# Kernel tuning notes

Measured on AMD Instinct MI355X. Metric: run time of the kernel, lower is better.

The kernel has to match this reference:

```python
import jax, jax.numpy as jnp
import numpy as np

B, L, C, H, W = 2, 4, 64, 80, 80
DISCRETE_RATIO, DOWNSAMPLE_RATE, NUM_ITER = 0.4, 2, 2


def _conv2d(x, w, b):
    y = jax.lax.conv_general_dilated(x, w, (1, 1), 'SAME',
                                     dimension_numbers=('NCHW', 'OIHW', 'NCHW'))
    return y + b[None, :, None, None]


def _get_transformation_matrix(M, h, w):
    # shift(center) @ [R 0; 0 1] @ shift(-center), then add raw translation (kornia-style)
    R = M[:, :2, :2]
    center = jnp.array([w / 2.0, h / 2.0], M.dtype)
    trans = center[None, :] - jnp.einsum('nij,j->ni', R, center) + M[:, :, 2]
    return jnp.concatenate([R, trans[:, :, None]], axis=2)  # (N,2,3)


def _warp_affine(src, M, mode):
    # src (N,C,h,w); M (N,2,3) maps src pixels -> dst pixels; sample src at M^{-1} @ dst
    # (equivalent to F.affine_grid/grid_sample with align_corners=True, zeros padding)
    N, Cc, h, w = src.shape
    bottom = jnp.tile(jnp.array([[[0.0, 0.0, 1.0]]], src.dtype), (N, 1, 1))
    Minv = jnp.linalg.inv(jnp.concatenate([M, bottom], axis=1))
    yy, xx = jnp.meshgrid(jnp.arange(h, dtype=src.dtype),
                          jnp.arange(w, dtype=src.dtype), indexing='ij')
    pts = jnp.stack([xx.ravel(), yy.ravel(), jnp.ones(h * w, src.dtype)], 0)  # (3,P)
    sp = jnp.einsum('nij,jp->nip', Minv, pts)
    sx, sy = sp[:, 0], sp[:, 1]  # (N,P) source pixel coords
    flat = src.reshape(N, Cc, h * w)

    def gather(ix, iy):
        valid = ((ix >= 0) & (ix < w) & (iy >= 0) & (iy < h)).astype(src.dtype)
        idx = jnp.clip(iy, 0, h - 1) * w + jnp.clip(ix, 0, w - 1)
        vals = jnp.take_along_axis(flat, jnp.broadcast_to(idx[:, None, :], (N, Cc, h * w)), axis=2)
        return vals * valid[:, None, :]

    if mode == 'nearest':
        out = gather(jnp.round(sx).astype(jnp.int32), jnp.round(sy).astype(jnp.int32))
    else:
        x0 = jnp.floor(sx); y0 = jnp.floor(sy)
        fx = (sx - x0)[:, None, :]; fy = (sy - y0)[:, None, :]
        x0 = x0.astype(jnp.int32); y0 = y0.astype(jnp.int32)
        out = (gather(x0, y0) * (1 - fx) * (1 - fy)
               + gather(x0 + 1, y0) * fx * (1 - fy)
               + gather(x0, y0 + 1) * (1 - fx) * fy
               + gather(x0 + 1, y0 + 1) * fx * fy)
    return out.reshape(N, Cc, h, w)


def _forward(x, pairwise_t_matrix, msg_w, msg_b, gates_w, gates_b, can_w, can_b, mlp_w, mlp_b):
    feats = x.reshape(B, L, C, H, W)
    # rows [0,1], cols [0,1,3] of the 4x4 SE(3) matrices; discretize translation
    t = pairwise_t_matrix[..., :2, :][..., jnp.array([0, 1, 3])]  # (B,L,L,2,3)
    t = t.at[..., 2].set(t[..., 2] / (DISCRETE_RATIO * DOWNSAMPLE_RATE))
    T = _get_transformation_matrix(t.reshape(-1, 2, 3), H, W)  # (B*L*L,2,3), flat index (b, j, i)
    mask = _warp_affine(jnp.ones((B * L * L, 1, H, W), x.dtype), T, 'nearest').reshape(B, L, L, 1, H, W)

    for _ in range(NUM_ITER):
        # 'b c h w -> b c w h' + flip(last): coordinate-convention fix (H==W)
        y = jnp.flip(jnp.swapaxes(feats, -1, -2), axis=-1)  # (B,L,C,H,W)
        # warp neighbor j into ego i frame with T[b,j,i]
        src = jnp.broadcast_to(y[:, :, None], (B, L, L, C, H, W)).reshape(-1, C, H, W)
        neighbor = _warp_affine(src, T, 'bilinear')
        ego = jnp.broadcast_to(y[:, None], (B, L, L, C, H, W)).reshape(-1, C, H, W)
        msg = _conv2d(jnp.concatenate([neighbor, ego], axis=1), msg_w, msg_b)
        msg = msg.reshape(B, L, L, C, H, W) * mask
        agg = msg.mean(axis=1)  # 'avg' over neighbors j -> (B,L,C,H,W)
        cat_feat = jnp.concatenate([y, agg], axis=2).reshape(B * L, 2 * C, H, W)
        # single ConvGRU step with zero initial hidden state
        h0 = jnp.zeros((B * L, C, H, W), x.dtype)
        gates = _conv2d(jnp.concatenate([cat_feat, h0], axis=1), gates_w, gates_b)
        reset = jax.nn.sigmoid(gates[:, :C])
        update = jax.nn.sigmoid(gates[:, C:])
        cand = jnp.tanh(_conv2d(jnp.concatenate([cat_feat, reset * h0], axis=1), can_w, can_b))
        h1 = (1.0 - update) * h0 + update * cand
        # undo the coordinate fix: flip(last) then 'c w h -> c h w'
        feats = jnp.swapaxes(jnp.flip(h1.reshape(B, L, C, H, W), axis=-1), -1, -2)

    out = feats[:, 0]  # ego agent of each sample, (B,C,H,W)
    return jnp.einsum('bchw,oc->bhwo', out, mlp_w) + mlp_b  # nn.Linear on channel-last


def setup_inputs() -> dict:
    key = jax.random.key(0)
    ks = jax.random.split(key, 12)
    x = jax.random.normal(ks[0], (B * L, C, H, W), dtype=jnp.float32)
    record_len = jnp.full((B,), L, dtype=jnp.int32)
    # realistic SE(2) pairwise transforms embedded in 4x4 homogeneous matrices
    ang = jax.random.uniform(ks[1], (B, L, L), minval=-0.3, maxval=0.3)
    tx = jax.random.uniform(ks[2], (B, L, L), minval=-8.0, maxval=8.0)
    ty = jax.random.uniform(ks[3], (B, L, L), minval=-8.0, maxval=8.0)
    c, s = jnp.cos(ang), jnp.sin(ang)
    z, o = jnp.zeros_like(ang), jnp.ones_like(ang)
    pairwise_t_matrix = jnp.stack([c, -s, z, tx,
                                   s, c, z, ty,
                                   z, z, o, z,
                                   z, z, z, o], axis=-1).reshape(B, L, L, 4, 4).astype(jnp.float32)
    prior_encoding = jax.random.normal(ks[4], (B * L, 3), dtype=jnp.float32)  # unused by forward
    sc = 0.05
    return {
        'x': x,
        'record_len': record_len,
        'pairwise_t_matrix': pairwise_t_matrix,
        'prior_encoding': prior_encoding,
        'msg_w': jax.random.normal(ks[5], (C, 2 * C, 3, 3), dtype=jnp.float32) * sc,
        'msg_b': jnp.zeros((C,), jnp.float32),
        'gates_w': jax.random.normal(ks[6], (2 * C, 3 * C, 3, 3), dtype=jnp.float32) * sc,
        'gates_b': jnp.zeros((2 * C,), jnp.float32),
        'can_w': jax.random.normal(ks[7], (C, 3 * C, 3, 3), dtype=jnp.float32) * sc,
        'can_b': jnp.zeros((C,), jnp.float32),
        'mlp_w': jax.random.normal(ks[8], (C, C), dtype=jnp.float32) * sc,
        'mlp_b': jnp.zeros((C,), jnp.float32),
    }


def reference(x, record_len, pairwise_t_matrix, prior_encoding,
              msg_w, msg_b, gates_w, gates_b, can_w, can_b, mlp_w, mlp_b):
    # record_len is fixed to L for every sample; prior_encoding is unused by the torch forward
    return _forward(x, pairwise_t_matrix, msg_w, msg_b, gates_w, gates_b,
                    can_w, can_b, mlp_w, mlp_b)
```

## Files before the change

kernel.cpp:

```cpp
#include <hip/hip_runtime.h>
#include <math.h>

#define WD 80
#define HW 6400
#define PW 82
#define PPX 6790
#define NIMG 8
#define NPAIR 32
#define RR 2
#define STG 640

typedef short bf16x8 __attribute__((ext_vector_type(8)));
typedef float f32x4 __attribute__((ext_vector_type(4)));

__device__ __forceinline__ float bf2f(unsigned short u) {
    return __uint_as_float(((unsigned)u) << 16);
}
__device__ __forceinline__ unsigned short f2bf(float f) {
    unsigned u = __float_as_uint(f);
    u += 0x7fff + ((u >> 16) & 1);
    return (unsigned short)(u >> 16);
}

__device__ __forceinline__ void inv_affine(const float* __restrict__ P, int p, float* a) {
    const float* m = P + p * 16;
    float m00 = m[0], m01 = m[1], m02 = m[3] / 0.8f;
    float m10 = m[4], m11 = m[5], m12 = m[7] / 0.8f;
    float cx = 40.0f, cy = 40.0f;
    float tx = cx - (m00 * cx + m01 * cy) + m02;
    float ty = cy - (m10 * cx + m11 * cy) + m12;
    float id = 1.0f / (m00 * m11 - m01 * m10);
    a[0] =  m11 * id; a[1] = -m01 * id;
    a[3] = -m10 * id; a[4] =  m00 * id;
    a[2] = -(a[0] * tx + a[1] * ty);
    a[5] = -(a[3] * tx + a[4] * ty);
}

__global__ void make_mask2(const float* __restrict__ P, float* __restrict__ mats,
                           float* __restrict__ mask) {
    int p = blockIdx.x;
    float a[6];
    inv_affine(P, p, a);
    if (threadIdx.x < 6) mats[p * 6 + threadIdx.x] = a[threadIdx.x];
    for (int q = threadIdx.x; q < HW; q += blockDim.x) {
        float x = (float)(q % WD), y = (float)(q / WD);
        float sx = a[0] * x + a[1] * y + a[2];
        float sy = a[3] * x + a[4] * y + a[5];
        int ix = (int)rintf(sx), iy = (int)rintf(sy);
        mask[p * HW + q] = (ix >= 0 && ix < WD && iy >= 0 && iy < WD) ? 1.0f : 0.0f;
    }
}

__global__ void zero_u4(uint4* __restrict__ p, int n4) {
    int t = blockIdx.x * blockDim.x + threadIdx.x;
    if (t < n4) p[t] = (uint4){0, 0, 0, 0};
}

__global__ __launch_bounds__(256) void rot_init_t(const float* __restrict__ x,
                                                  unsigned short* __restrict__ Y) {
    __shared__ float T[64][81];
    int img = blockIdx.x / 80, hh = blockIdx.x % 80;
    int tid = threadIdx.x;
    for (int idx = tid; idx < 64 * 80; idx += 256) {
        int c = idx / 80, ww = idx % 80;
        T[c][ww] = x[((size_t)(img * 64 + c) * 80 + hh) * 80 + ww];
    }
    __syncthreads();
    int b = 79 - hh;
    for (int idx = tid; idx < 80 * 64; idx += 256) {
        int a = idx >> 6, ch = idx & 63;
        Y[((size_t)img * PPX + (a + 1) * PW + (b + 1)) * 64 + ch] = f2bf(T[ch][a]);
    }
}

__global__ void prep_w_all(const float* __restrict__ msg_w, const float* __restrict__ gates_w,
                           const float* __restrict__ can_w,
                           unsigned short* __restrict__ Wn, unsigned short* __restrict__ We,
                           unsigned short* __restrict__ Wu, unsigned short* __restrict__ Wc) {
    int t = blockIdx.x * blockDim.x + threadIdx.x;
    if (t >= 221184) return;
    const float* src; unsigned short* dst;
    int cin_n, co_off, ci_off, stride, u;
    if (t < 36864)       { src = msg_w;   dst = Wn; cin_n = 64;  co_off = 0;  ci_off = 0;  stride = 1152; u = t; }
    else if (t < 73728)  { src = msg_w;   dst = We; cin_n = 64;  co_off = 0;  ci_off = 64; stride = 1152; u = t - 36864; }
    else if (t < 147456) { src = gates_w; dst = Wu; cin_n = 128; co_off = 64; ci_off = 0;  stride = 1728; u = t - 73728; }
    else                 { src = can_w;   dst = Wc; cin_n = 128; co_off = 0;  ci_off = 0;  stride = 1728; u = t - 147456; }
    int ci = u % cin_n;
    int co = (u / cin_n) & 63;
    int tap = u / (cin_n * 64);
    dst[u] = f2bf(src[(size_t)(co_off + co) * stride + (ci_off + ci) * 9 + tap]);
}

__global__ void warp_pairs(const unsigned short* __restrict__ Ysrc, const float* __restrict__ mats,
                           unsigned short* __restrict__ warped, int total, int only0) {
    int idx = blockIdx.x * blockDim.x + threadIdx.x;
    if (idx >= total) return;
    int g = idx & 7;
    int pp = (idx >> 3) % 6724;
    int k = idx / (6724 * 8);
    int p = only0 ? k * 4 : k;
    int py = pp / PW, pxx = pp % PW;
    uint4 v = {0, 0, 0, 0};
    if (py >= 1 && py <= 80 && pxx >= 1 && pxx <= 80) {
        int y = py - 1, x = pxx - 1;
        const float* a = mats + p * 6;
        float sx = a[0] * x + a[1] * y + a[2];
        float sy = a[3] * x + a[4] * y + a[5];
        float fxf = floorf(sx), fyf = floorf(sy);
        float fx = sx - fxf, fy = sy - fyf;
        int ix = (int)fxf, iy = (int)fyf;
        float w00 = (1.f - fx) * (1.f - fy), w10 = fx * (1.f - fy);
        float w01 = (1.f - fx) * fy,         w11 = fx * fy;
        bool vx0 = (unsigned)ix < WD, vx1 = (unsigned)(ix + 1) < WD;
        bool vy0 = (unsigned)iy < WD, vy1 = (unsigned)(iy + 1) < WD;
        if (!(vx0 && vy0)) w00 = 0.f;
        if (!(vx1 && vy0)) w10 = 0.f;
        if (!(vx0 && vy1)) w01 = 0.f;
        if (!(vx1 && vy1)) w11 = 0.f;
        int cx0 = min(max(ix, 0), WD - 1), cx1 = min(max(ix + 1, 0), WD - 1);
        int cy0 = min(max(iy, 0), WD - 1), cy1 = min(max(iy + 1, 0), WD - 1);
        const unsigned short* src = Ysrc + (size_t)(p >> 2) * PPX * 64 + g * 8;
        uint4 c00 = *(const uint4*)(src + ((cy0 + 1) * PW + cx0 + 1) * 64);
        uint4 c10 = *(const uint4*)(src + ((cy0 + 1) * PW + cx1 + 1) * 64);
        uint4 c01 = *(const uint4*)(src + ((cy1 + 1) * PW + cx0 + 1) * 64);
        uint4 c11 = *(const uint4*)(src + ((cy1 + 1) * PW + cx1 + 1) * 64);
        const unsigned short* p00 = (const unsigned short*)&c00;
        const unsigned short* p10 = (const unsigned short*)&c10;
        const unsigned short* p01 = (const unsigned short*)&c01;
        const unsigned short* p11 = (const unsigned short*)&c11;
        unsigned short r8[8];
#pragma unroll
        for (int kk = 0; kk < 8; ++kk) {
            float vv = w00 * bf2f(p00[kk]) + w10 * bf2f(p10[kk])
                     + w01 * bf2f(p01[kk]) + w11 * bf2f(p11[kk]);
            r8[kk] = f2bf(vv);
        }
        v = *(const uint4*)r8;
    }
    *(uint4*)(warped + ((size_t)k * PPX + pp) * 64 + g * 8) = v;
}

__device__ __forceinline__ void stage_t(const unsigned short* __restrict__ src,
                                        int x0, int y0, uint4* bufbase, int tid) {
    const int lane = tid & 63;
    const int wv = tid >> 6;
    for (int c = wv; c < STG / 64; c += 4) {
        int s = c * 64 + lane;
        int q = s >> 3;
        int yl = q / 20, xl = q - yl * 20;
        int g = (s & 7) ^ (q & 7);
        const unsigned short* gp = src + ((y0 + yl) * PW + x0 + xl) * 64 + g * 8;
        __builtin_amdgcn_global_load_lds(
            (const __attribute__((address_space(1))) unsigned int*)gp,
            (__attribute__((address_space(3))) unsigned int*)(bufbase + c * 64),
            16, 0, 0);
    }
}

__device__ __forceinline__ void load_w(const unsigned short* __restrict__ W, int row,
                                       int cinstride, int cin0, int lh, bf16x8* Wf) {
#pragma unroll
    for (int ks = 0; ks < 2; ++ks)
#pragma unroll
        for (int tap = 0; tap < 9; ++tap)
            Wf[ks * 9 + tap] = *(const bf16x8*)(W + (size_t)(tap * 64 + row) * cinstride
                                                + cin0 + ks * 32 + lh * 8);
}

__device__ __forceinline__ void conv_pass(const uint4* __restrict__ buf, const bf16x8* Wf,
                                          int ll, int lh, f32x4* acc) {
#pragma unroll
    for (int ks = 0; ks < 2; ++ks) {
        int g = ks * 4 + lh;
#pragma unroll
        for (int tap = 0; tap < 9; ++tap) {
            bf16x8 B = Wf[ks * 9 + tap];
            int ty = tap / 3, tx = tap % 3;
#pragma unroll
            for (int r = 0; r < RR; ++r) {
                int q = (r + ty) * 20 + tx + ll;
                bf16x8 A = *(const bf16x8*)&buf[q * 8 + (g ^ (q & 7))];
                acc[r] = __builtin_amdgcn_mfma_f32_16x16x32_bf16(A, B, acc[r], 0, 0, 0);
            }
        }
    }
}

__global__ __launch_bounds__(256) void msg_agg(const unsigned short* __restrict__ warped,
        const unsigned short* __restrict__ Y, const float* __restrict__ mask,
        const unsigned short* __restrict__ Wn, const unsigned short* __restrict__ We,
        const float* __restrict__ bias, unsigned short* __restrict__ Gpad, int only0) {
    __shared__ uint4 lds[2 * STG];
    __shared__ float lmask[4][RR][16];
    const int tid = threadIdx.x, lane = tid & 63, wv = tid >> 6;
    const int ll = lane & 15, lh = lane >> 4;
    const int x0 = blockIdx.x * 16, y0 = blockIdx.y * RR;
    const int t = blockIdx.z;
    const int b = only0 ? t : (t >> 2), j = only0 ? 0 : (t & 3);
    const int row = wv * 16 + ll;
    const int img = only0 ? t * 4 : t;

    int ks_[4];
#pragma unroll
    for (int i = 0; i < 4; ++i)
        ks_[i] = only0 ? (b * 4 + i) : ((b * 4 + i) * 4 + j);
    if (tid < 4 * RR * 16) {
        int i = tid / (RR * 16), r = (tid >> 4) % RR, px = tid & 15;
        int p = only0 ? ks_[i] * 4 : ks_[i];
        lmask[i][r][px] = mask[(size_t)p * HW + (y0 + r) * WD + x0 + px];
    }
    bf16x8 Wf[18];
    load_w(Wn, row, 64, 0, lh, Wf);
    stage_t(warped + (size_t)ks_[0] * PPX * 64, x0, y0, lds, tid);
    __syncthreads();

    f32x4 tot[RR];
#pragma unroll
    for (int r = 0; r < RR; ++r) tot[r] = (f32x4){0.f, 0.f, 0.f, 0.f};

    for (int i = 0; i < 4; ++i) {
        if (i < 3)
            stage_t(warped + (size_t)ks_[i + 1] * PPX * 64, x0, y0, lds + ((i + 1) & 1) * STG, tid);
        else
            stage_t(Y + (size_t)img * PPX * 64, x0, y0, lds, tid);
        f32x4 acc[RR];
#pragma unroll
        for (int r = 0; r < RR; ++r) acc[r] = (f32x4){0.f, 0.f, 0.f, 0.f};
        conv_pass(lds + (i & 1) * STG, Wf, ll, lh, acc);
#pragma unroll
        for (int r = 0; r < RR; ++r)
#pragma unroll
            for (int jj = 0; jj < 4; ++jj)
                tot[r][jj] += lmask[i][r][lh * 4 + jj] * acc[r][jj];
        __syncthreads();
    }

    load_w(We, row, 64, 0, lh, Wf);
    f32x4 acc[RR];
#pragma unroll
    for (int r = 0; r < RR; ++r) acc[r] = (f32x4){0.f, 0.f, 0.f, 0.f};
    conv_pass(lds, Wf, ll, lh, acc);

    float bv = bias[row];
#pragma unroll
    for (int r = 0; r < RR; ++r)
#pragma unroll
        for (int jj = 0; jj < 4; ++jj) {
            int px = lh * 4 + jj;
            float msum = lmask[0][r][px] + lmask[1][r][px] + lmask[2][r][px] + lmask[3][r][px];
            float val = 0.25f * (tot[r][jj] + msum * (acc[r][jj] + bv));
            Gpad[((size_t)t * PPX + (y0 + r + 1) * PW + (x0 + px + 1)) * 64 + row] = f2bf(val);
        }
}

__global__ __launch_bounds__(256) void gru_conv(const unsigned short* __restrict__ Ysrc,
        const unsigned short* __restrict__ Gpad,
        const unsigned short* __restrict__ Wu, const unsigned short* __restrict__ Wc,
        const float* __restrict__ bu, const float* __restrict__ bc,
        unsigned short* __restrict__ Ydst, int only0) {
    __shared__ uint4 lds[2 * STG];
    const int tid = threadIdx.x, lane = tid & 63, wv = tid >> 6;
    const int ll = lane & 15, lh = lane >> 4;
    const int x0 = blockIdx.x * 16, y0 = blockIdx.y * RR;
    const int t = blockIdx.z;
    const int img = only0 ? t * 4 : t;
    const int row = wv * 16 + ll;

    stage_t(Ysrc + (size_t)img * PPX * 64, x0, y0, lds, tid);
    stage_t(Gpad + (size_t)t * PPX * 64, x0, y0, lds + STG, tid);
    bf16x8 Wf[18];
    load_w(Wu, row, 128, 0, lh, Wf);
    __syncthreads();

    f32x4 aU[RR], aC[RR];
#pragma unroll
    for (int r = 0; r < RR; ++r) {
        aU[r] = (f32x4){0.f, 0.f, 0.f, 0.f};
        aC[r] = (f32x4){0.f, 0.f, 0.f, 0.f};
    }
    conv_pass(lds, Wf, ll, lh, aU);
    load_w(Wu, row, 128, 64, lh, Wf);
    conv_pass(lds + STG, Wf, ll, lh, aU);
    load_w(Wc, row, 128, 0, lh, Wf);
    conv_pass(lds, Wf, ll, lh, aC);
    load_w(Wc, row, 128, 64, lh, Wf);
    conv_pass(lds + STG, Wf, ll, lh, aC);

    float ub = bu[row], cb = bc[row];
#pragma unroll
    for (int r = 0; r < RR; ++r)
#pragma unroll
        for (int jj = 0; jj < 4; ++jj) {
            float u = 1.f / (1.f + __expf(-(aU[r][jj] + ub)));
            float e2 = __expf(2.f * (aC[r][jj] + cb));
            float c = (e2 - 1.f) / (e2 + 1.f);
            Ydst[((size_t)img * PPX + (y0 + r + 1) * PW + (x0 + lh * 4 + jj + 1)) * 64 + row]
                = f2bf(u * c);
        }
}

__global__ void final_mlp(const unsigned short* __restrict__ yfin, const float* __restrict__ mw,
                          const float* __restrict__ mb, float* __restrict__ out) {
    int t = blockIdx.x * blockDim.x + threadIdx.x;
    if (t >= 2 * HW * 64) return;
    int o  = t & 63;
    int wv = (t >> 6) % WD;
    int h  = ((t >> 6) / WD) % WD;
    int b  = t / (HW * 64);
    const unsigned short* src = yfin + ((size_t)(b * 4) * PPX + (wv + 1) * PW + (80 - h)) * 64;
    const float* wrow = mw + o * 64;
    float r = mb[o];
#pragma unroll
    for (int c8 = 0; c8 < 8; ++c8) {
        bf16x8 v = *(const bf16x8*)(src + c8 * 8);
#pragma unroll
        for (int k = 0; k < 8; ++k)
            r += bf2f(((const unsigned short*)&v)[k]) * wrow[c8 * 8 + k];
    }
    out[t] = r;
}

extern "C" void kernel_launch(void* const* d_in, const int* in_sizes, int n_in,
                              void* d_out, int out_size, void* d_ws, size_t ws_size,
                              hipStream_t stream) {
    const float* x       = (const float*)d_in[0];
    const float* P       = (const float*)d_in[2];
    const float* msg_w   = (const float*)d_in[4];
    const float* msg_b   = (const float*)d_in[5];
    const float* gates_w = (const float*)d_in[6];
    const float* gates_b = (const float*)d_in[7];
    const float* can_w   = (const float*)d_in[8];
    const float* can_b   = (const float*)d_in[9];
    const float* mlp_w   = (const float*)d_in[10];
    const float* mlp_b   = (const float*)d_in[11];
    float* out = (float*)d_out;

    char* wsb = (char*)d_ws;
    float* mats = (float*)wsb;
    float* mask = (float*)(wsb + 1024);
    unsigned short* Wn = (unsigned short*)(wsb + 820224);
    unsigned short* We = Wn + 36864;
    unsigned short* Wu = We + 36864;
    unsigned short* Wc = Wu + 73728;
    unsigned short* Y0 = Wc + 73728;
    unsigned short* Y1 = Y0 + (size_t)NIMG * PPX * 64;
    unsigned short* Gpad = Y1 + (size_t)NIMG * PPX * 64;
    unsigned short* warped = Gpad + (size_t)NIMG * PPX * 64;

    {
        int n4 = (int)((size_t)3 * NIMG * PPX * 64 * 2 / 16);
        zero_u4<<<(n4 + 255) / 256, 256, 0, stream>>>((uint4*)Y0, n4);
    }
    make_mask2<<<NPAIR, 256, 0, stream>>>(P, mats, mask);
    prep_w_all<<<(221184 + 255) / 256, 256, 0, stream>>>(msg_w, gates_w, can_w, Wn, We, Wu, Wc);
    rot_init_t<<<NIMG * 80, 256, 0, stream>>>(x, Y0);

    warp_pairs<<<(32 * 6724 * 8 + 255) / 256, 256, 0, stream>>>(Y0, mats, warped, 32 * 6724 * 8, 0);
    msg_agg<<<dim3(5, 80 / RR, 8), 256, 0, stream>>>(warped, Y0, mask, Wn, We, msg_b, Gpad, 0);
    gru_conv<<<dim3(5, 80 / RR, 8), 256, 0, stream>>>(Y0, Gpad, Wu, Wc, gates_b + 64, can_b, Y1, 0);

    warp_pairs<<<(8 * 6724 * 8 + 255) / 256, 256, 0, stream>>>(Y1, mats, warped, 8 * 6724 * 8, 1);
    msg_agg<<<dim3(5, 80 / RR, 2), 256, 0, stream>>>(warped, Y1, mask, Wn, We, msg_b, Gpad, 1);
    gru_conv<<<dim3(5, 80 / RR, 2), 256, 0, stream>>>(Y1, Gpad, Wu, Wc, gates_b + 64, can_b, Y0, 1);

    final_mlp<<<(2 * HW * 64 + 255) / 256, 256, 0, stream>>>(Y0, mlp_w, mlp_b, out);
}
```

Measured before the change: 282.6 us.

## Enlarge conv tiles to 8 rows with warp row/channel split and A-fragment reuse

The conv kernels now process 8 output rows per block instead of 2. Each wave computes 4 rows by 32 output channels, and each loaded A fragment is reused across the 3 vertical taps and 2 channel groups. Weights are read from global/L1 inside the loop instead of being held in registers. This cuts halo restaging and LDS reads per output. The trade-offs are 4x fewer blocks (200 or 50 per launch), larger LDS usage, and more global weight loads in the inner loop.

```diff
diff --git a/kernel.cpp b/kernel.cpp
--- a/kernel.cpp
+++ b/kernel.cpp
@@ -7,8 +7,8 @@
 #define PPX 6790
 #define NIMG 8
 #define NPAIR 32
-#define RR 2
-#define STG 640
+#define YR 8
+#define TSTG 1600
 
 typedef short bf16x8 __attribute__((ext_vector_type(8)));
 typedef float f32x4 __attribute__((ext_vector_type(4)));
@@ -144,7 +144,7 @@
                                         int x0, int y0, uint4* bufbase, int tid) {
     const int lane = tid & 63;
     const int wv = tid >> 6;
-    for (int c = wv; c < STG / 64; c += 4) {
+    for (int c = wv; c < TSTG / 64; c += 4) {
         int s = c * 64 + lane;
         int q = s >> 3;
         int yl = q / 20, xl = q - yl * 20;
@@ -157,146 +157,168 @@
     }
 }
 
-__device__ __forceinline__ void load_w(const unsigned short* __restrict__ W, int row,
-                                       int cinstride, int cin0, int lh, bf16x8* Wf) {
-#pragma unroll
-    for (int ks = 0; ks < 2; ++ks)
-#pragma unroll
-        for (int tap = 0; tap < 9; ++tap)
-            Wf[ks * 9 + tap] = *(const bf16x8*)(W + (size_t)(tap * 64 + row) * cinstride
+__device__ __forceinline__ void conv_pass(const uint4* __restrict__ buf,
+        const unsigned short* __restrict__ W, int cinstride, int cin0,
+        int ll, int lh, int rg, int cgp, f32x4 acc[2][4]) {
+#pragma unroll
+    for (int ks = 0; ks < 2; ++ks) {
+        const int g = ks * 4 + lh;
+#pragma unroll
+        for (int tx = 0; tx < 3; ++tx) {
+            bf16x8 A[6];
+#pragma unroll
+            for (int s = 0; s < 6; ++s) {
+                int q = (rg * 4 + s) * 20 + tx + ll;
+                A[s] = *(const bf16x8*)&buf[q * 8 + (g ^ (q & 7))];
+            }
+#pragma unroll
+            for (int ty = 0; ty < 3; ++ty) {
+                int tap = ty * 3 + tx;
+#pragma unroll
+                for (int c2 = 0; c2 < 2; ++c2) {
+                    int co = cgp * 32 + c2 * 16 + ll;
+                    bf16x8 B = *(const bf16x8*)(W + (size_t)(tap * 64 + co) * cinstride
                                                 + cin0 + ks * 32 + lh * 8);
-}
-
-__device__ __forceinline__ void conv_pass(const uint4* __restrict__ buf, const bf16x8* Wf,
-                                          int ll, int lh, f32x4* acc) {
-#pragma unroll
-    for (int ks = 0; ks < 2; ++ks) {
-        int g = ks * 4 + lh;
-#pragma unroll
-        for (int tap = 0; tap < 9; ++tap) {
-            bf16x8 B = Wf[ks * 9 + tap];
-            int ty = tap / 3, tx = tap % 3;
-#pragma unroll
-            for (int r = 0; r < RR; ++r) {
-                int q = (r + ty) * 20 + tx + ll;
-                bf16x8 A = *(const bf16x8*)&buf[q * 8 + (g ^ (q & 7))];
-                acc[r] = __builtin_amdgcn_mfma_f32_16x16x32_bf16(A, B, acc[r], 0, 0, 0);
-            }
-        }
-    }
-}
-
-__global__ __launch_bounds__(256) void msg_agg(const unsigned short* __restrict__ warped,
+#pragma unroll
+                    for (int r = 0; r < 4; ++r)
+                        acc[c2][r] = __builtin_amdgcn_mfma_f32_16x16x32_bf16(A[r + ty], B, acc[c2][r], 0, 0, 0);
+                }
+            }
+        }
+    }
+}
+
+__global__ __launch_bounds__(256, 3) void msg_agg(const unsigned short* __restrict__ warped,
         const unsigned short* __restrict__ Y, const float* __restrict__ mask,
         const unsigned short* __restrict__ Wn, const unsigned short* __restrict__ We,
         const float* __restrict__ bias, unsigned short* __restrict__ Gpad, int only0) {
-    __shared__ uint4 lds[2 * STG];
-    __shared__ float lmask[4][RR][16];
+    __shared__ uint4 lds[2 * TSTG];
+    __shared__ float lmask[4][YR][16];
     const int tid = threadIdx.x, lane = tid & 63, wv = tid >> 6;
     const int ll = lane & 15, lh = lane >> 4;
-    const int x0 = blockIdx.x * 16, y0 = blockIdx.y * RR;
+    const int rg = wv & 1, cgp = wv >> 1;
+    const int x0 = blockIdx.x * 16, y0 = blockIdx.y * YR;
     const int t = blockIdx.z;
     const int b = only0 ? t : (t >> 2), j = only0 ? 0 : (t & 3);
-    const int row = wv * 16 + ll;
     const int img = only0 ? t * 4 : t;
 
     int ks_[4];
 #pragma unroll
     for (int i = 0; i < 4; ++i)
         ks_[i] = only0 ? (b * 4 + i) : ((b * 4 + i) * 4 + j);
-    if (tid < 4 * RR * 16) {
-        int i = tid / (RR * 16), r = (tid >> 4) % RR, px = tid & 15;
+    for (int idx = tid; idx < 4 * YR * 16; idx += 256) {
+        int i = idx / (YR * 16), r = (idx >> 4) % YR, px = idx & 15;
         int p = only0 ? ks_[i] * 4 : ks_[i];
         lmask[i][r][px] = mask[(size_t)p * HW + (y0 + r) * WD + x0 + px];
     }
-    bf16x8 Wf[18];
-    load_w(Wn, row, 64, 0, lh, Wf);
     stage_t(warped + (size_t)ks_[0] * PPX * 64, x0, y0, lds, tid);
     __syncthreads();
 
-    f32x4 tot[RR];
-#pragma unroll
-    for (int r = 0; r < RR; ++r) tot[r] = (f32x4){0.f, 0.f, 0.f, 0.f};
+    f32x4 tot[2][4];
+    float msum[4][4];
+#pragma unroll
+    for (int c2 = 0; c2 < 2; ++c2)
+#pragma unroll
+        for (int r = 0; r < 4; ++r) tot[c2][r] = (f32x4){0.f, 0.f, 0.f, 0.f};
+#pragma unroll
+    for (int r = 0; r < 4; ++r)
+#pragma unroll
+        for (int jj = 0; jj < 4; ++jj) msum[r][jj] = 0.f;
 
     for (int i = 0; i < 4; ++i) {
         if (i < 3)
-            stage_t(warped + (size_t)ks_[i + 1] * PPX * 64, x0, y0, lds + ((i + 1) & 1) * STG, tid);
+            stage_t(warped + (size_t)ks_[i + 1] * PPX * 64, x0, y0, lds + ((i + 1) & 1) * TSTG, tid);
         else
             stage_t(Y + (size_t)img * PPX * 64, x0, y0, lds, tid);
-        f32x4 acc[RR];
-#pragma unroll
-        for (int r = 0; r < RR; ++r) acc[r] = (f32x4){0.f, 0.f, 0.f, 0.f};
-        conv_pass(lds + (i & 1) * STG, Wf, ll, lh, acc);
-#pragma unroll
-        for (int r = 0; r < RR; ++r)
-#pragma unroll
-            for (int jj = 0; jj < 4; ++jj)
-                tot[r][jj] += lmask[i][r][lh * 4 + jj] * acc[r][jj];
+        f32x4 acc[2][4];
+#pragma unroll
+        for (int c2 = 0; c2 < 2; ++c2)
+#pragma unroll
+            for (int r = 0; r < 4; ++r) acc[c2][r] = (f32x4){0.f, 0.f, 0.f, 0.f};
+        conv_pass(lds + (i & 1) * TSTG, Wn, 64, 0, ll, lh, rg, cgp, acc);
+#pragma unroll
+        for (int r = 0; r < 4; ++r)
+#pragma unroll
+            for (int jj = 0; jj < 4; ++jj) {
+                float m = lmask[i][rg * 4 + r][lh * 4 + jj];
+                msum[r][jj] += m;
+#pragma unroll
+                for (int c2 = 0; c2 < 2; ++c2) tot[c2][r][jj] += m * acc[c2][r][jj];
+            }
         __syncthreads();
     }
 
-    load_w(We, row, 64, 0, lh, Wf);
-    f32x4 acc[RR];
-#pragma unroll
-    for (int r = 0; r < RR; ++r) acc[r] = (f32x4){0.f, 0.f, 0.f, 0.f};
-    conv_pass(lds, Wf, ll, lh, acc);
-
-    float bv = bias[row];
-#pragma unroll
-    for (int r = 0; r < RR; ++r)
-#pragma unroll
-        for (int jj = 0; jj < 4; ++jj) {
-            int px = lh * 4 + jj;
-            float msum = lmask[0][r][px] + lmask[1][r][px] + lmask[2][r][px] + lmask[3][r][px];
-            float val = 0.25f * (tot[r][jj] + msum * (acc[r][jj] + bv));
-            Gpad[((size_t)t * PPX + (y0 + r + 1) * PW + (x0 + px + 1)) * 64 + row] = f2bf(val);
-        }
-}
-
-__global__ __launch_bounds__(256) void gru_conv(const unsigned short* __restrict__ Ysrc,
+    f32x4 acc[2][4];
+#pragma unroll
+    for (int c2 = 0; c2 < 2; ++c2)
+#pragma unroll
+        for (int r = 0; r < 4; ++r) acc[c2][r] = (f32x4){0.f, 0.f, 0.f, 0.f};
+    conv_pass(lds, We, 64, 0, ll, lh, rg, cgp, acc);
+
+#pragma unroll
+    for (int c2 = 0; c2 < 2; ++c2) {
+        int co = cgp * 32 + c2 * 16 + ll;
+        float bv = bias[co];
+#pragma unroll
+        for (int r = 0; r < 4; ++r) {
+            int y = y0 + rg * 4 + r;
+#pragma unroll
+            for (int jj = 0; jj < 4; ++jj) {
+                int x = x0 + lh * 4 + jj;
+                float val = 0.25f * (tot[c2][r][jj] + msum[r][jj] * (acc[c2][r][jj] + bv));
+                Gpad[((size_t)t * PPX + (y + 1) * PW + (x + 1)) * 64 + co] = f2bf(val);
+            }
+        }
+    }
+}
+
+__global__ __launch_bounds__(256, 3) void gru_conv(const unsigned short* __restrict__ Ysrc,
         const unsigned short* __restrict__ Gpad,
         const unsigned short* __restrict__ Wu, const unsigned short* __restrict__ Wc,
         const float* __restrict__ bu, const float* __restrict__ bc,
         unsigned short* __restrict__ Ydst, int only0) {
-    __shared__ uint4 lds[2 * STG];
+    __shared__ uint4 lds[2 * TSTG];
     const int tid = threadIdx.x, lane = tid & 63, wv = tid >> 6;
     const int ll = lane & 15, lh = lane >> 4;
-    const int x0 = blockIdx.x * 16, y0 = blockIdx.y * RR;
+    const int rg = wv & 1, cgp = wv >> 1;
+    const int x0 = blockIdx.x * 16, y0 = blockIdx.y * YR;
     const int t = blockIdx.z;
     const int img = only0 ? t * 4 : t;
-    const int row = wv * 16 + ll;
 
     stage_t(Ysrc + (size_t)img * PPX * 64, x0, y0, lds, tid);
-    stage_t(Gpad + (size_t)t * PPX * 64, x0, y0, lds + STG, tid);
-    bf16x8 Wf[18];
-    load_w(Wu, row, 128, 0, lh, Wf);
+    stage_t(Gpad + (size_t)t * PPX * 64, x0, y0, lds + TSTG, tid);
     __syncthreads();
 
-    f32x4 aU[RR], aC[RR];
-#pragma unroll
-    for (int r = 0; r < RR; ++r) {
-        aU[r] = (f32x4){0.f, 0.f, 0.f, 0.f};
-        aC[r] = (f32x4){0.f, 0.f, 0.f, 0.f};
-    }
-    conv_pass(lds, Wf, ll, lh, aU);
-    load_w(Wu, row, 128, 64, lh, Wf);
-    conv_pass(lds + STG, Wf, ll, lh, aU);
-    load_w(Wc, row, 128, 0, lh, Wf);
-    conv_pass(lds, Wf, ll, lh, aC);
-    load_w(Wc, row, 128, 64, lh, Wf);
-    conv_pass(lds + STG, Wf, ll, lh, aC);
-
-    float ub = bu[row], cb = bc[row];
-#pragma unroll
-    for (int r = 0; r < RR; ++r)
-#pragma unroll
-        for (int jj = 0; jj < 4; ++jj) {
-            float u = 1.f / (1.f + __expf(-(aU[r][jj] + ub)));
-            float e2 = __expf(2.f * (aC[r][jj] + cb));
-            float c = (e2 - 1.f) / (e2 + 1.f);
-            Ydst[((size_t)img * PPX + (y0 + r + 1) * PW + (x0 + lh * 4 + jj + 1)) * 64 + row]
-                = f2bf(u * c);
-        }
+    f32x4 aU[2][4], aC[2][4];
+#pragma unroll
+    for (int c2 = 0; c2 < 2; ++c2)
+#pragma unroll
+        for (int r = 0; r < 4; ++r) {
+            aU[c2][r] = (f32x4){0.f, 0.f, 0.f, 0.f};
+            aC[c2][r] = (f32x4){0.f, 0.f, 0.f, 0.f};
+        }
+    conv_pass(lds,        Wu, 128, 0,  ll, lh, rg, cgp, aU);
+    conv_pass(lds + TSTG, Wu, 128, 64, ll, lh, rg, cgp, aU);
+    conv_pass(lds,        Wc, 128, 0,  ll, lh, rg, cgp, aC);
+    conv_pass(lds + TSTG, Wc, 128, 64, ll, lh, rg, cgp, aC);
+
+#pragma unroll
+    for (int c2 = 0; c2 < 2; ++c2) {
+        int co = cgp * 32 + c2 * 16 + ll;
+        float ub = bu[co], cb = bc[co];
+#pragma unroll
+        for (int r = 0; r < 4; ++r) {
+            int y = y0 + rg * 4 + r;
+#pragma unroll
+            for (int jj = 0; jj < 4; ++jj) {
+                int x = x0 + lh * 4 + jj;
+                float u = 1.f / (1.f + __expf(-(aU[c2][r][jj] + ub)));
+                float e2 = __expf(2.f * (aC[c2][r][jj] + cb));
+                float c = (e2 - 1.f) / (e2 + 1.f);
+                Ydst[((size_t)img * PPX + (y + 1) * PW + (x + 1)) * 64 + co] = f2bf(u * c);
+            }
+        }
+    }
 }
 
 __global__ void final_mlp(const unsigned short* __restrict__ yfin, const float* __restrict__ mw,
@@ -356,12 +378,12 @@
     rot_init_t<<<NIMG * 80, 256, 0, stream>>>(x, Y0);
 
     warp_pairs<<<(32 * 6724 * 8 + 255) / 256, 256, 0, stream>>>(Y0, mats, warped, 32 * 6724 * 8, 0);
-    msg_agg<<<dim3(5, 80 / RR, 8), 256, 0, stream>>>(warped, Y0, mask, Wn, We, msg_b, Gpad, 0);
-    gru_conv<<<dim3(5, 80 / RR, 8), 256, 0, stream>>>(Y0, Gpad, Wu, Wc, gates_b + 64, can_b, Y1, 0);
+    msg_agg<<<dim3(5, 80 / YR, 8), 256, 0, stream>>>(warped, Y0, mask, Wn, We, msg_b, Gpad, 0);
+    gru_conv<<<dim3(5, 80 / YR, 8), 256, 0, stream>>>(Y0, Gpad, Wu, Wc, gates_b + 64, can_b, Y1, 0);
 
     warp_pairs<<<(8 * 6724 * 8 + 255) / 256, 256, 0, stream>>>(Y1, mats, warped, 8 * 6724 * 8, 1);
-    msg_agg<<<dim3(5, 80 / RR, 2), 256, 0, stream>>>(warped, Y1, mask, Wn, We, msg_b, Gpad, 1);
-    gru_conv<<<dim3(5, 80 / RR, 2), 256, 0, stream>>>(Y1, Gpad, Wu, Wc, gates_b + 64, can_b, Y0, 1);
+    msg_agg<<<dim3(5, 80 / YR, 2), 256, 0, stream>>>(warped, Y1, mask, Wn, We, msg_b, Gpad, 1);
+    gru_conv<<<dim3(5, 80 / YR, 2), 256, 0, stream>>>(Y1, Gpad, Wu, Wc, gates_b + 64, can_b, Y0, 1);
 
     final_mlp<<<(2 * HW * 64 + 255) / 256, 256, 0, stream>>>(Y0, mlp_w, mlp_b, out);
 }
```

New measurement: 395.1 us. 1.4x slower.

## Enlarge conv tiles to four rows with register-reused A fragments and fused prologue

Applied to the files above, without the earlier changes.

Each conv block now covers four output rows instead of two, and staged LDS tiles grow to match. The inner loop loads six A fragments per column tap and reuses each across the three row taps, which cuts LDS reads per MFMA. gru_conv double-buffers its weight fragments so the next weight load overlaps the current pass. The mask and weight-prep kernels are merged into one prologue launch, and both conv kernels get a launch bound of two blocks per SIMD. In exchange there are half as many blocks, which may lower occupancy and latency hiding, and register pressure rises.

```diff
diff --git a/kernel.cpp b/kernel.cpp
--- a/kernel.cpp
+++ b/kernel.cpp
@@ -7,8 +7,7 @@
 #define PPX 6790
 #define NIMG 8
 #define NPAIR 32
-#define RR 2
-#define STG 640
+#define TSTG 960
 
 typedef short bf16x8 __attribute__((ext_vector_type(8)));
 typedef float f32x4 __attribute__((ext_vector_type(4)));
@@ -36,48 +35,28 @@
     a[5] = -(a[3] * tx + a[4] * ty);
 }
 
-__global__ void make_mask2(const float* __restrict__ P, float* __restrict__ mats,
-                           float* __restrict__ mask) {
-    int p = blockIdx.x;
-    float a[6];
-    inv_affine(P, p, a);
-    if (threadIdx.x < 6) mats[p * 6 + threadIdx.x] = a[threadIdx.x];
-    for (int q = threadIdx.x; q < HW; q += blockDim.x) {
-        float x = (float)(q % WD), y = (float)(q / WD);
-        float sx = a[0] * x + a[1] * y + a[2];
-        float sy = a[3] * x + a[4] * y + a[5];
-        int ix = (int)rintf(sx), iy = (int)rintf(sy);
-        mask[p * HW + q] = (ix >= 0 && ix < WD && iy >= 0 && iy < WD) ? 1.0f : 0.0f;
-    }
-}
-
-__global__ void zero_u4(uint4* __restrict__ p, int n4) {
-    int t = blockIdx.x * blockDim.x + threadIdx.x;
-    if (t < n4) p[t] = (uint4){0, 0, 0, 0};
-}
-
-__global__ __launch_bounds__(256) void rot_init_t(const float* __restrict__ x,
-                                                  unsigned short* __restrict__ Y) {
-    __shared__ float T[64][81];
-    int img = blockIdx.x / 80, hh = blockIdx.x % 80;
-    int tid = threadIdx.x;
-    for (int idx = tid; idx < 64 * 80; idx += 256) {
-        int c = idx / 80, ww = idx % 80;
-        T[c][ww] = x[((size_t)(img * 64 + c) * 80 + hh) * 80 + ww];
-    }
-    __syncthreads();
-    int b = 79 - hh;
-    for (int idx = tid; idx < 80 * 64; idx += 256) {
-        int a = idx >> 6, ch = idx & 63;
-        Y[((size_t)img * PPX + (a + 1) * PW + (b + 1)) * 64 + ch] = f2bf(T[ch][a]);
-    }
-}
-
-__global__ void prep_w_all(const float* __restrict__ msg_w, const float* __restrict__ gates_w,
-                           const float* __restrict__ can_w,
-                           unsigned short* __restrict__ Wn, unsigned short* __restrict__ We,
-                           unsigned short* __restrict__ Wu, unsigned short* __restrict__ Wc) {
-    int t = blockIdx.x * blockDim.x + threadIdx.x;
+__global__ void prologue(const float* __restrict__ P, float* __restrict__ mats,
+                         float* __restrict__ mask,
+                         const float* __restrict__ msg_w, const float* __restrict__ gates_w,
+                         const float* __restrict__ can_w,
+                         unsigned short* __restrict__ Wn, unsigned short* __restrict__ We,
+                         unsigned short* __restrict__ Wu, unsigned short* __restrict__ Wc) {
+    int bx = blockIdx.x;
+    if (bx < 32) {
+        int p = bx;
+        float a[6];
+        inv_affine(P, p, a);
+        if (threadIdx.x < 6) mats[p * 6 + threadIdx.x] = a[threadIdx.x];
+        for (int q = threadIdx.x; q < HW; q += blockDim.x) {
+            float x = (float)(q % WD), y = (float)(q / WD);
+            float sx = a[0] * x + a[1] * y + a[2];
+            float sy = a[3] * x + a[4] * y + a[5];
+            int ix = (int)rintf(sx), iy = (int)rintf(sy);
+            mask[p * HW + q] = (ix >= 0 && ix < WD && iy >= 0 && iy < WD) ? 1.0f : 0.0f;
+        }
+        return;
+    }
+    int t = (bx - 32) * 256 + threadIdx.x;
     if (t >= 221184) return;
     const float* src; unsigned short* dst;
     int cin_n, co_off, ci_off, stride, u;
@@ -89,6 +68,28 @@
     int co = (u / cin_n) & 63;
     int tap = u / (cin_n * 64);
     dst[u] = f2bf(src[(size_t)(co_off + co) * stride + (ci_off + ci) * 9 + tap]);
+}
+
+__global__ void zero_u4(uint4* __restrict__ p, int n4) {
+    int t = blockIdx.x * blockDim.x + threadIdx.x;
+    if (t < n4) p[t] = (uint4){0, 0, 0, 0};
+}
+
+__global__ __launch_bounds__(256) void rot_init_t(const float* __restrict__ x,
+                                                  unsigned short* __restrict__ Y) {
+    __shared__ float T[64][81];
+    int img = blockIdx.x / 80, hh = blockIdx.x % 80;
+    int tid = threadIdx.x;
+    for (int idx = tid; idx < 64 * 80; idx += 256) {
+        int c = idx / 80, ww = idx % 80;
+        T[c][ww] = x[((size_t)(img * 64 + c) * 80 + hh) * 80 + ww];
+    }
+    __syncthreads();
+    int b = 79 - hh;
+    for (int idx = tid; idx < 80 * 64; idx += 256) {
+        int a = idx >> 6, ch = idx & 63;
+        Y[((size_t)img * PPX + (a + 1) * PW + (b + 1)) * 64 + ch] = f2bf(T[ch][a]);
+    }
 }
 
 __global__ void warp_pairs(const unsigned short* __restrict__ Ysrc, const float* __restrict__ mats,
@@ -144,7 +145,7 @@
                                         int x0, int y0, uint4* bufbase, int tid) {
     const int lane = tid & 63;
     const int wv = tid >> 6;
-    for (int c = wv; c < STG / 64; c += 4) {
+    for (int c = wv; c < TSTG / 64; c += 4) {
         int s = c * 64 + lane;
         int q = s >> 3;
         int yl = q / 20, xl = q - yl * 20;
@@ -167,45 +168,50 @@
                                                 + cin0 + ks * 32 + lh * 8);
 }
 
-__device__ __forceinline__ void conv_pass(const uint4* __restrict__ buf, const bf16x8* Wf,
-                                          int ll, int lh, f32x4* acc) {
+__device__ __forceinline__ void conv_pass4(const uint4* __restrict__ buf, const bf16x8* Wf,
+                                           int ll, int lh, f32x4* acc) {
 #pragma unroll
     for (int ks = 0; ks < 2; ++ks) {
-        int g = ks * 4 + lh;
-#pragma unroll
-        for (int tap = 0; tap < 9; ++tap) {
-            bf16x8 B = Wf[ks * 9 + tap];
-            int ty = tap / 3, tx = tap % 3;
-#pragma unroll
-            for (int r = 0; r < RR; ++r) {
-                int q = (r + ty) * 20 + tx + ll;
-                bf16x8 A = *(const bf16x8*)&buf[q * 8 + (g ^ (q & 7))];
-                acc[r] = __builtin_amdgcn_mfma_f32_16x16x32_bf16(A, B, acc[r], 0, 0, 0);
+        const int g = ks * 4 + lh;
+#pragma unroll
+        for (int tx = 0; tx < 3; ++tx) {
+            bf16x8 A[6];
+#pragma unroll
+            for (int s = 0; s < 6; ++s) {
+                int q = s * 20 + tx + ll;
+                A[s] = *(const bf16x8*)&buf[q * 8 + (g ^ (q & 7))];
             }
-        }
-    }
-}
-
-__global__ __launch_bounds__(256) void msg_agg(const unsigned short* __restrict__ warped,
+#pragma unroll
+            for (int ty = 0; ty < 3; ++ty) {
+                bf16x8 B = Wf[ks * 9 + ty * 3 + tx];
+#pragma unroll
+                for (int r = 0; r < 4; ++r)
+                    acc[r] = __builtin_amdgcn_mfma_f32_16x16x32_bf16(A[r + ty], B, acc[r], 0, 0, 0);
+            }
+        }
+    }
+}
+
+__global__ __launch_bounds__(256, 2) void msg_agg(const unsigned short* __restrict__ warped,
         const unsigned short* __restrict__ Y, const float* __restrict__ mask,
         const unsigned short* __restrict__ Wn, const unsigned short* __restrict__ We,
         const float* __restrict__ bias, unsigned short* __restrict__ Gpad, int only0) {
-    __shared__ uint4 lds[2 * STG];
-    __shared__ float lmask[4][RR][16];
+    __shared__ uint4 lds[2 * TSTG];
+    __shared__ float lmask[4][4][16];
     const int tid = threadIdx.x, lane = tid & 63, wv = tid >> 6;
     const int ll = lane & 15, lh = lane >> 4;
-    const int x0 = blockIdx.x * 16, y0 = blockIdx.y * RR;
+    const int x0 = blockIdx.x * 16, y0 = blockIdx.y * 4;
     const int t = blockIdx.z;
     const int b = only0 ? t : (t >> 2), j = only0 ? 0 : (t & 3);
+    const int img = only0 ? t * 4 : t;
     const int row = wv * 16 + ll;
-    const int img = only0 ? t * 4 : t;
 
     int ks_[4];
 #pragma unroll
     for (int i = 0; i < 4; ++i)
         ks_[i] = only0 ? (b * 4 + i) : ((b * 4 + i) * 4 + j);
-    if (tid < 4 * RR * 16) {
-        int i = tid / (RR * 16), r = (tid >> 4) % RR, px = tid & 15;
+    {
+        int i = tid >> 6, r = (tid >> 4) & 3, px = tid & 15;
         int p = only0 ? ks_[i] * 4 : ks_[i];
         lmask[i][r][px] = mask[(size_t)p * HW + (y0 + r) * WD + x0 + px];
     }
@@ -214,88 +220,95 @@
     stage_t(warped + (size_t)ks_[0] * PPX * 64, x0, y0, lds, tid);
     __syncthreads();
 
-    f32x4 tot[RR];
-#pragma unroll
-    for (int r = 0; r < RR; ++r) tot[r] = (f32x4){0.f, 0.f, 0.f, 0.f};
+    f32x4 tot[4];
+    float msum[4][4];
+#pragma unroll
+    for (int r = 0; r < 4; ++r) {
+        tot[r] = (f32x4){0.f, 0.f, 0.f, 0.f};
+#pragma unroll
+        for (int jj = 0; jj < 4; ++jj) msum[r][jj] = 0.f;
+    }
 
     for (int i = 0; i < 4; ++i) {
         if (i < 3)
-            stage_t(warped + (size_t)ks_[i + 1] * PPX * 64, x0, y0, lds + ((i + 1) & 1) * STG, tid);
+            stage_t(warped + (size_t)ks_[i + 1] * PPX * 64, x0, y0, lds + ((i + 1) & 1) * TSTG, tid);
         else
             stage_t(Y + (size_t)img * PPX * 64, x0, y0, lds, tid);
-        f32x4 acc[RR];
-#pragma unroll
-        for (int r = 0; r < RR; ++r) acc[r] = (f32x4){0.f, 0.f, 0.f, 0.f};
-        conv_pass(lds + (i & 1) * STG, Wf, ll, lh, acc);
-#pragma unroll
-        for (int r = 0; r < RR; ++r)
-#pragma unroll
-            for (int jj = 0; jj < 4; ++jj)
-                tot[r][jj] += lmask[i][r][lh * 4 + jj] * acc[r][jj];
+        f32x4 acc[4];
+#pragma unroll
+        for (int r = 0; r < 4; ++r) acc[r] = (f32x4){0.f, 0.f, 0.f, 0.f};
+        conv_pass4(lds + (i & 1) * TSTG, Wf, ll, lh, acc);
+#pragma unroll
+        for (int r = 0; r < 4; ++r)
+#pragma unroll
+            for (int jj = 0; jj < 4; ++jj) {
+                float m = lmask[i][r][lh * 4 + jj];
+                msum[r][jj] += m;
+                tot[r][jj] += m * acc[r][jj];
+            }
         __syncthreads();
     }
 
     load_w(We, row, 64, 0, lh, Wf);
-    f32x4 acc[RR];
-#pragma unroll
-    for (int r = 0; r < RR; ++r) acc[r] = (f32x4){0.f, 0.f, 0.f, 0.f};
-    conv_pass(lds, Wf, ll, lh, acc);
+    f32x4 acc[4];
+#pragma unroll
+    for (int r = 0; r < 4; ++r) acc[r] = (f32x4){0.f, 0.f, 0.f, 0.f};
+    conv_pass4(lds, Wf, ll, lh, acc);
 
     float bv = bias[row];
 #pragma unroll
-    for (int r = 0; r < RR; ++r)
+    for (int r = 0; r < 4; ++r)
 #pragma unroll
         for (int jj = 0; jj < 4; ++jj) {
-            int px = lh * 4 + jj;
-            float msum = lmask[0][r][px] + lmask[1][r][px] + lmask[2][r][px] + lmask[3][r][px];
-            float val = 0.25f * (tot[r][jj] + msum * (acc[r][jj] + bv));
-            Gpad[((size_t)t * PPX + (y0 + r + 1) * PW + (x0 + px + 1)) * 64 + row] = f2bf(val);
-        }
-}
-
-__global__ __launch_bounds__(256) void gru_conv(const unsigned short* __restrict__ Ysrc,
+            int x = x0 + lh * 4 + jj;
+            float val = 0.25f * (tot[r][jj] + msum[r][jj] * (acc[r][jj] + bv));
+            Gpad[((size_t)t * PPX + (y0 + r + 1) * PW + (x + 1)) * 64 + row] = f2bf(val);
+        }
+}
+
+__global__ __launch_bounds__(256, 2) void gru_conv(const unsigned short* __restrict__ Ysrc,
         const unsigned short* __restrict__ Gpad,
         const unsigned short* __restrict__ Wu, const unsigned short* __restrict__ Wc,
         const float* __restrict__ bu, const float* __restrict__ bc,
         unsigned short* __restrict__ Ydst, int only0) {
-    __shared__ uint4 lds[2 * STG];
+    __shared__ uint4 lds[2 * TSTG];
     const int tid = threadIdx.x, lane = tid & 63, wv = tid >> 6;
     const int ll = lane & 15, lh = lane >> 4;
-    const int x0 = blockIdx.x * 16, y0 = blockIdx.y * RR;
+    const int x0 = blockIdx.x * 16, y0 = blockIdx.y * 4;
     const int t = blockIdx.z;
     const int img = only0 ? t * 4 : t;
     const int row = wv * 16 + ll;
 
     stage_t(Ysrc + (size_t)img * PPX * 64, x0, y0, lds, tid);
-    stage_t(Gpad + (size_t)t * PPX * 64, x0, y0, lds + STG, tid);
-    bf16x8 Wf[18];
-    load_w(Wu, row, 128, 0, lh, Wf);
+    stage_t(Gpad + (size_t)t * PPX * 64, x0, y0, lds + TSTG, tid);
+    bf16x8 W0[18], W1[18];
+    load_w(Wu, row, 128, 0,  lh, W0);
+    load_w(Wu, row, 128, 64, lh, W1);
     __syncthreads();
 
-    f32x4 aU[RR], aC[RR];
-#pragma unroll
-    for (int r = 0; r < RR; ++r) {
+    f32x4 aU[4], aC[4];
+#pragma unroll
+    for (int r = 0; r < 4; ++r) {
         aU[r] = (f32x4){0.f, 0.f, 0.f, 0.f};
         aC[r] = (f32x4){0.f, 0.f, 0.f, 0.f};
     }
-    conv_pass(lds, Wf, ll, lh, aU);
-    load_w(Wu, row, 128, 64, lh, Wf);
-    conv_pass(lds + STG, Wf, ll, lh, aU);
-    load_w(Wc, row, 128, 0, lh, Wf);
-    conv_pass(lds, Wf, ll, lh, aC);
-    load_w(Wc, row, 128, 64, lh, Wf);
-    conv_pass(lds + STG, Wf, ll, lh, aC);
+    conv_pass4(lds,        W0, ll, lh, aU);
+    load_w(Wc, row, 128, 0,  lh, W0);
+    conv_pass4(lds + TSTG, W1, ll, lh, aU);
+    load_w(Wc, row, 128, 64, lh, W1);
+    conv_pass4(lds,        W0, ll, lh, aC);
+    conv_pass4(lds + TSTG, W1, ll, lh, aC);
 
     float ub = bu[row], cb = bc[row];
 #pragma unroll
-    for (int r = 0; r < RR; ++r)
+    for (int r = 0; r < 4; ++r)
 #pragma unroll
         for (int jj = 0; jj < 4; ++jj) {
+            int x = x0 + lh * 4 + jj;
             float u = 1.f / (1.f + __expf(-(aU[r][jj] + ub)));
             float e2 = __expf(2.f * (aC[r][jj] + cb));
             float c = (e2 - 1.f) / (e2 + 1.f);
-            Ydst[((size_t)img * PPX + (y0 + r + 1) * PW + (x0 + lh * 4 + jj + 1)) * 64 + row]
-                = f2bf(u * c);
+            Ydst[((size_t)img * PPX + (y0 + r + 1) * PW + (x + 1)) * 64 + row] = f2bf(u * c);
         }
 }
 
@@ -351,17 +364,17 @@
         int n4 = (int)((size_t)3 * NIMG * PPX * 64 * 2 / 16);
         zero_u4<<<(n4 + 255) / 256, 256, 0, stream>>>((uint4*)Y0, n4);
     }
-    make_mask2<<<NPAIR, 256, 0, stream>>>(P, mats, mask);
-    prep_w_all<<<(221184 + 255) / 256, 256, 0, stream>>>(msg_w, gates_w, can_w, Wn, We, Wu, Wc);
+    prologue<<<32 + (221184 + 255) / 256, 256, 0, stream>>>(P, mats, mask,
+        msg_w, gates_w, can_w, Wn, We, Wu, Wc);
     rot_init_t<<<NIMG * 80, 256, 0, stream>>>(x, Y0);
 
     warp_pairs<<<(32 * 6724 * 8 + 255) / 256, 256, 0, stream>>>(Y0, mats, warped, 32 * 6724 * 8, 0);
-    msg_agg<<<dim3(5, 80 / RR, 8), 256, 0, stream>>>(warped, Y0, mask, Wn, We, msg_b, Gpad, 0);
-    gru_conv<<<dim3(5, 80 / RR, 8), 256, 0, stream>>>(Y0, Gpad, Wu, Wc, gates_b + 64, can_b, Y1, 0);
+    msg_agg<<<dim3(5, 20, 8), 256, 0, stream>>>(warped, Y0, mask, Wn, We, msg_b, Gpad, 0);
+    gru_conv<<<dim3(5, 20, 8), 256, 0, stream>>>(Y0, Gpad, Wu, Wc, gates_b + 64, can_b, Y1, 0);
 
     warp_pairs<<<(8 * 6724 * 8 + 255) / 256, 256, 0, stream>>>(Y1, mats, warped, 8 * 6724 * 8, 1);
-    msg_agg<<<dim3(5, 80 / RR, 2), 256, 0, stream>>>(warped, Y1, mask, Wn, We, msg_b, Gpad, 1);
-    gru_conv<<<dim3(5, 80 / RR, 2), 256, 0, stream>>>(Y1, Gpad, Wu, Wc, gates_b + 64, can_b, Y0, 1);
+    msg_agg<<<dim3(5, 20, 2), 256, 0, stream>>>(warped, Y1, mask, Wn, We, msg_b, Gpad, 1);
+    gru_conv<<<dim3(5, 20, 2), 256, 0, stream>>>(Y1, Gpad, Wu, Wc, gates_b + 64, can_b, Y0, 1);
 
     final_mlp<<<(2 * HW * 64 + 255) / 256, 256, 0, stream>>>(Y0, mlp_w, mlp_b, out);
 }
```

Measured after the change: 247.3 us. 1.14x faster.
